# Performance work log

Hardware: AMD Instinct MI355X
Metric: run time of the kernel (lower is better)

## Reference

```python
import jax, jax.numpy as jnp
import numpy as np

N = 50000          # num nodes
E = 800000         # edges per adjacency
NUM_A = 4          # number of adjacency matrices
C = 2              # num_channels
D_IN = 128
D_OUT = 64


def setup_inputs() -> dict:
    key = jax.random.key(0)
    k1, k2, k3, k4, k5, k6 = jax.random.split(key, 6)
    H = jax.random.normal(k1, (N, D_IN), dtype=jnp.float32)
    vals = jax.random.uniform(k2, (NUM_A, E), dtype=jnp.float32)
    rows = jax.random.randint(k3, (NUM_A, E), 0, N, dtype=jnp.int32)
    cols = jax.random.randint(k4, (NUM_A, E), 0, N, dtype=jnp.int32)
    # xavier-ish init for learned params
    weight = jax.random.normal(k5, (C, D_IN, D_OUT), dtype=jnp.float32) * (2.0 / (D_IN + D_OUT)) ** 0.5
    att_weight = jax.random.normal(k6, (C, D_IN, NUM_A), dtype=jnp.float32) * (2.0 / (D_IN + NUM_A)) ** 0.5
    return {"H": H, "vals": vals, "weight": weight, "att_weight": att_weight,
            "rows": rows, "cols": cols}


def reference(H, vals, weight, att_weight, rows, cols):
    # H: [N, in], weight: [C, in, out], att_weight: [C, in, num_A]
    # rows/cols/vals: [num_A, E] COO edge lists for each sparse adjacency A_i
    n = H.shape[0]
    num_channels = weight.shape[0]
    Hc_all = jnp.einsum('nd,cdo->cno', H, weight)            # [C, N, out]
    score = jax.nn.softmax(att_weight.mean(axis=1), axis=1)   # [C, num_A]
    r = rows.reshape(-1)                                      # [num_A*E]
    cl = cols.reshape(-1)
    outs = []
    for c in range(num_channels):
        # A_combined = sum_i score[c, i] * A_i, applied as SpMM via segment_sum
        w = (score[c][:, None] * vals).reshape(-1)            # [num_A*E]
        msgs = Hc_all[c][cl] * w[:, None]                     # [num_A*E, out]
        outs.append(jax.ops.segment_sum(msgs, r, num_segments=n))
    return jnp.mean(jnp.stack(outs, axis=0), axis=0)          # [N, out]
```

## Files before the change

### kernel.cpp

```cpp
#include <hip/hip_runtime.h>
#include <hip/hip_fp16.h>

constexpr int D_IN  = 128;
constexpr int D_OUT = 64;
constexpr int NCH   = 2;
constexpr int NUM_A = 4;
constexpr int COLS  = NCH * D_OUT;
constexpr int RPB   = 64;
constexpr int MAXNB = 800;
constexpr int CAP   = 4608;
constexpr int SPT   = 512;
constexpr int RPT   = CAP / SPT;
constexpr int CAPB  = 6144;

typedef __attribute__((ext_vector_type(8))) short bf16x8;
typedef __attribute__((ext_vector_type(4))) float f32x4;

__device__ inline unsigned short f2bf_rn(float f) {
    unsigned u = __float_as_uint(f);
    return (unsigned short)((u + 0x7fffu + ((u >> 16) & 1u)) >> 16);
}
__device__ inline unsigned short f2h(float f) {
    _Float16 h = (_Float16)f;
    unsigned short u; __builtin_memcpy(&u, &h, 2); return u;
}
__device__ inline __half2 u2h2(unsigned u) {
    __half2 h; __builtin_memcpy(&h, &u, 4); return h;
}

__global__ __launch_bounds__(64) void score_kernel(const float* __restrict__ att,
                                                   float* __restrict__ score,
                                                   unsigned* __restrict__ cinit,
                                                   int NB, int padded) {
    int lane = threadIdx.x;
    for (int i = lane; i < NB; i += 64)
        cinit[i] = padded ? (unsigned)i * (unsigned)CAPB : 0u;
    int c = lane >> 2, a = lane & 3;
    float s = 0.0f;
    if (lane < 8) {
        const float* p = att + c * (D_IN * NUM_A) + a;
        for (int d = 0; d < D_IN; ++d) s += p[d * NUM_A];
        s *= (1.0f / D_IN);
    }
    float m = fmaxf(s, __shfl_xor(s, 1));
    m = fmaxf(m, __shfl_xor(m, 2));
    float ex = __expf(s - m);
    float sum = ex + __shfl_xor(ex, 1);
    sum += __shfl_xor(sum, 2);
    if (lane < 8) score[lane] = 0.5f * ex / sum;
}

__global__ __launch_bounds__(256) void gemm_kernel(const float* __restrict__ H,
                                                   const float* __restrict__ W,
                                                   unsigned short* __restrict__ Hc, int N) {
    __shared__ unsigned short Bs[128 * 136];

    const int t = threadIdx.x;
    for (int i = t; i < 128 * 128; i += 256) {
        const int k = i >> 7, n = i & 127;
        const int c = n >> 6, nn = n & 63;
        Bs[n * 136 + k] = f2bf_rn(W[c * (D_IN * D_OUT) + k * D_OUT + nn]);
    }

    const int lane = t & 63;
    const int wr   = t >> 6;
    const int kg   = lane >> 4;
    const int l15  = lane & 15;
    const int row0 = blockIdx.x * 64;

    int arow = row0 + wr * 16 + l15;
    if (arow >= N) arow = N - 1;

    bf16x8 afrag[4];
    const float* hrow = H + (size_t)arow * D_IN;
    #pragma unroll
    for (int s = 0; s < 4; ++s) {
        const int k0 = s * 32 + kg * 8;
        const float4 f0 = *reinterpret_cast<const float4*>(hrow + k0);
        const float4 f1 = *reinterpret_cast<const float4*>(hrow + k0 + 4);
        bf16x8 av;
        av[0] = (short)f2bf_rn(f0.x); av[1] = (short)f2bf_rn(f0.y);
        av[2] = (short)f2bf_rn(f0.z); av[3] = (short)f2bf_rn(f0.w);
        av[4] = (short)f2bf_rn(f1.x); av[5] = (short)f2bf_rn(f1.y);
        av[6] = (short)f2bf_rn(f1.z); av[7] = (short)f2bf_rn(f1.w);
        afrag[s] = av;
    }
    __syncthreads();

    #pragma unroll
    for (int nt = 0; nt < 8; ++nt) {
        const int n = nt * 16 + l15;
        f32x4 acc = {0.f, 0.f, 0.f, 0.f};
        #pragma unroll
        for (int s = 0; s < 4; ++s) {
            const bf16x8 bfrag =
                *reinterpret_cast<const bf16x8*>(&Bs[n * 136 + s * 32 + kg * 8]);
            acc = __builtin_amdgcn_mfma_f32_16x16x32_bf16(afrag[s], bfrag, acc, 0, 0, 0);
        }
        #pragma unroll
        for (int r = 0; r < 4; ++r) {
            const int drow = row0 + wr * 16 + kg * 4 + r;
            if (drow < N) Hc[(size_t)drow * COLS + n] = f2h(acc[r]);
        }
    }
}

__global__ __launch_bounds__(1024) void hist_kernel(const int* __restrict__ rows,
                                                    unsigned* __restrict__ counts,
                                                    int TE, int NB) {
    __shared__ unsigned h[MAXNB];
    const int t = threadIdx.x;
    for (int i = t; i < MAXNB; i += 1024) h[i] = 0u;
    __syncthreads();
    for (int e = blockIdx.x * 1024 + t; e < TE; e += gridDim.x * 1024)
        atomicAdd(&h[rows[e] >> 6], 1u);
    __syncthreads();
    for (int i = t; i < NB; i += 1024)
        if (h[i]) atomicAdd(&counts[i], h[i]);
}

__global__ __launch_bounds__(1024) void scan_kernel(const unsigned* __restrict__ counts,
                                                    unsigned* __restrict__ offsets,
                                                    unsigned* __restrict__ cursor, int n) {
    __shared__ unsigned part[1024];
    const int t = threadIdx.x;
    const int chunk = (n + 1023) >> 10;
    const int s = t * chunk;
    const int e = min(s + chunk, n);
    unsigned sum = 0;
    for (int i = s; i < e; ++i) sum += counts[i];
    part[t] = sum;
    __syncthreads();
    for (int d = 1; d < 1024; d <<= 1) {
        unsigned v = (t >= d) ? part[t - d] : 0u;
        __syncthreads();
        part[t] += v;
        __syncthreads();
    }
    unsigned run = (t == 0) ? 0u : part[t - 1];
    for (int i = s; i < e; ++i) {
        const unsigned c = counts[i];
        offsets[i] = run;
        cursor[i]  = run;
        run += c;
    }
}

constexpr int SC_T   = 1024;
constexpr int SC_EPT = 6;
constexpr int SC_CH  = SC_T * SC_EPT;

__global__ __launch_bounds__(SC_T) void scatter_kernel(const int* __restrict__ rows,
                                                       const int* __restrict__ cols,
                                                       const float* __restrict__ vals,
                                                       const float* __restrict__ score,
                                                       unsigned* __restrict__ cursor,
                                                       uint2* __restrict__ erec,
                                                       int TE, int Eper, int NB) {
    __shared__ unsigned lh[MAXNB];
    __shared__ unsigned lbase[MAXNB];
    __shared__ unsigned gbase[MAXNB];
    __shared__ unsigned wsum[16];
    __shared__ __align__(16) uint2 srec[SC_CH];
    __shared__ float ssc[8];

    const int t  = threadIdx.x;
    const int e0 = blockIdx.x * SC_CH;

    if (t < 8) ssc[t] = score[t];
    for (int i = t; i < MAXNB; i += SC_T) lh[i] = 0u;
    __syncthreads();

    unsigned bkrank[SC_EPT], meta[SC_EPT], wpk[SC_EPT];
    #pragma unroll
    for (int k = 0; k < SC_EPT; ++k) {
        const int e = e0 + k * SC_T + t;
        bkrank[k] = 0xffffffffu;
        if (e < TE) {
            const int row = rows[e];
            const int col = cols[e];
            const float v = vals[e];
            const int  a  = e / Eper;
            const unsigned bk = (unsigned)(row >> 6);
            const unsigned rk = atomicAdd(&lh[bk], 1u);
            bkrank[k] = (bk << 16) | rk;
            meta[k]   = (unsigned)col | ((unsigned)(row & 63) << 16) | (bk << 22);
            wpk[k]    = (unsigned)f2h(ssc[a] * v) |
                        ((unsigned)f2h(ssc[4 + a] * v) << 16);
        }
    }
    __syncthreads();

    const unsigned v = (t < NB) ? lh[t] : 0u;
    unsigned incl = v;
    #pragma unroll
    for (int d = 1; d < 64; d <<= 1) {
        const unsigned nb = __shfl_up(incl, d);
        if ((t & 63) >= d) incl += nb;
    }
    if ((t & 63) == 63) wsum[t >> 6] = incl;
    __syncthreads();
    if (t < 16) {
        const unsigned s = wsum[t];
        unsigned i2 = s;
        #pragma unroll
        for (int d = 1; d < 16; d <<= 1) {
            const unsigned nb = __shfl_up(i2, d);
            if (t >= d) i2 += nb;
        }
        wsum[t] = i2 - s;
    }
    __syncthreads();
    if (t < NB) {
        lbase[t] = incl - v + wsum[t >> 6];
        gbase[t] = v ? atomicAdd(&cursor[t], v) : 0u;
    }
    __syncthreads();

    #pragma unroll
    for (int k = 0; k < SC_EPT; ++k) {
        if (bkrank[k] != 0xffffffffu) {
            const unsigned p = lbase[bkrank[k] >> 16] + (bkrank[k] & 0xffffu);
            srec[p] = make_uint2(meta[k], wpk[k]);
        }
    }
    __syncthreads();

    const unsigned cn = min((unsigned)(TE - e0), (unsigned)SC_CH);
    #pragma unroll
    for (int k = 0; k < SC_EPT; ++k) {
        const unsigned p = (unsigned)(k * SC_T + t);
        if (p < cn) {
            const uint2 r = srec[p];
            const unsigned bk = r.x >> 22;
            const unsigned dst = gbase[bk] + (p - lbase[bk]);
            erec[dst] = make_uint2(r.x & 0x003fffffu, r.y);
        }
    }
}

__global__ __launch_bounds__(SPT) void bucketspmm_kernel(const uint2* __restrict__ erec,
                                                         const unsigned* __restrict__ offsets,
                                                         const unsigned* __restrict__ counts,
                                                         const unsigned* __restrict__ cursor,
                                                         const unsigned* __restrict__ Hc32,
                                                         float* __restrict__ out,
                                                         int N, int padded) {
    __shared__ __align__(16) uint2 srec[CAP];
    __shared__ unsigned roff8[8 * 68];
    __shared__ unsigned roff[RPB + 1];

    const int t    = threadIdx.x;
    const int lane = t & 63;
    const int w    = t >> 6;
    const int bucket = blockIdx.x;
    unsigned start, cnt;
    if (padded) {
        start = (unsigned)bucket * (unsigned)CAPB;
        cnt   = cursor[bucket] - start;
    } else {
        start = offsets[bucket];
        cnt   = counts[bucket];
    }
    const unsigned psel = (lane < 32) ? 0x01000100u : 0x03020302u;

    float2 acc[8];
    #pragma unroll
    for (int r = 0; r < 8; ++r) acc[r] = make_float2(0.f, 0.f);

    for (unsigned cb = 0; cb < cnt; cb += CAP) {
        const unsigned cn = min(cnt - cb, (unsigned)CAP);

        for (int i = t; i < 8 * 68; i += SPT) roff8[i] = 0u;
        __syncthreads();

        uint2 rec[RPT];
        unsigned rank[RPT];
        #pragma unroll
        for (int k = 0; k < RPT; ++k) {
            const unsigned idx = (unsigned)(k * SPT + t);
            rec[k] = make_uint2(0xffffffffu, 0u);
            if (idx < cn) {
                rec[k] = erec[start + cb + idx];
                rank[k] = atomicAdd(&roff8[w * 68 + (rec[k].x >> 16)], 1u);
            }
        }
        __syncthreads();

        if (t < 64) {
            unsigned run = 0;
            #pragma unroll
            for (int w2 = 0; w2 < 8; ++w2) {
                const unsigned v = roff8[w2 * 68 + t];
                roff8[w2 * 68 + t] = run;
                run += v;
            }
            unsigned incl = run;
            #pragma unroll
            for (int d = 1; d < 64; d <<= 1) {
                const unsigned nb = __shfl_up(incl, d);
                if (lane >= d) incl += nb;
            }
            roff[t] = incl - run;
            if (t == 63) roff[RPB] = incl;
        }
        __syncthreads();

        #pragma unroll
        for (int k = 0; k < RPT; ++k) {
            if (rec[k].x != 0xffffffffu) {
                const unsigned rib = rec[k].x >> 16;
                const unsigned pos = roff[rib] + roff8[w * 68 + rib] + rank[k];
                srec[pos] = make_uint2(rec[k].x & 0xffffu, rec[k].y);
            }
        }
        __syncthreads();

        #pragma unroll
        for (int rr = 0; rr < 8; ++rr) {
            const int r = w * 8 + rr;
            unsigned j = roff[r];
            const unsigned e = roff[r + 1];
            float2 a = acc[rr];

            while (j + 16 <= e) {
                unsigned hv16[16], wv16[16];
                #pragma unroll
                for (int k = 0; k < 16; ++k) {
                    const uint2 rc = srec[j + k];
                    hv16[k] = Hc32[(rc.x << 6) + lane];
                    wv16[k] = __builtin_amdgcn_perm(rc.y, rc.y, psel);
                }
                __half2 h2a = u2h2(0u), h2b = u2h2(0u);
                #pragma unroll
                for (int k = 0; k < 16; k += 2) {
                    h2a = __hfma2(u2h2(hv16[k]),     u2h2(wv16[k]),     h2a);
                    h2b = __hfma2(u2h2(hv16[k + 1]), u2h2(wv16[k + 1]), h2b);
                }
                const __half2 hs = __hadd2(h2a, h2b);
                a.x += __low2float(hs);
                a.y += __high2float(hs);
                j += 16;
            }
            if (j < e) {
                __half2 h2 = u2h2(0u);
                while (j + 4 <= e) {
                    unsigned hv4[4], wv4[4];
                    #pragma unroll
                    for (int k = 0; k < 4; ++k) {
                        const uint2 rc = srec[j + k];
                        hv4[k] = Hc32[(rc.x << 6) + lane];
                        wv4[k] = __builtin_amdgcn_perm(rc.y, rc.y, psel);
                    }
                    #pragma unroll
                    for (int k = 0; k < 4; ++k)
                        h2 = __hfma2(u2h2(hv4[k]), u2h2(wv4[k]), h2);
                    j += 4;
                }
                for (; j < e; ++j) {
                    const uint2 rc = srec[j];
                    const unsigned hv = Hc32[(rc.x << 6) + lane];
                    const unsigned wv = __builtin_amdgcn_perm(rc.y, rc.y, psel);
                    h2 = __hfma2(u2h2(hv), u2h2(wv), h2);
                }
                a.x += __low2float(h2);
                a.y += __high2float(h2);
            }
            acc[rr] = a;
        }
        __syncthreads();
    }

    const int row0 = bucket * RPB + w * 8;
    #pragma unroll
    for (int rr = 0; rr < 8; ++rr) {
        float2 a = acc[rr];
        a.x += __shfl_xor(a.x, 32);
        a.y += __shfl_xor(a.y, 32);
        const int row = row0 + rr;
        if (lane < 32 && row < N) {
            *reinterpret_cast<float2*>(out + (size_t)row * D_OUT + lane * 2) = a;
        }
    }
}

extern "C" void kernel_launch(void* const* d_in, const int* in_sizes, int n_in,
                              void* d_out, int out_size, void* d_ws, size_t ws_size,
                              hipStream_t stream) {
    const float* H    = (const float*)d_in[0];
    const float* vals = (const float*)d_in[1];
    const float* W    = (const float*)d_in[2];
    const float* att  = (const float*)d_in[3];
    const int*   rows = (const int*)d_in[4];
    const int*   cols = (const int*)d_in[5];

    const int N    = in_sizes[0] / D_IN;
    const int TE   = in_sizes[1];
    const int Eper = TE / NUM_A;
    const int NB   = (N + RPB - 1) / RPB;

    char* ws = (char*)d_ws;
    size_t off = 0;
    float* ws_score = (float*)(ws + off);          off += 256;
    unsigned short* ws_Hc = (unsigned short*)(ws + off);
    off += (size_t)N * COLS * sizeof(unsigned short);
    off = (off + 255) & ~(size_t)255;
    unsigned* counts  = (unsigned*)(ws + off);     off += (size_t)MAXNB * sizeof(unsigned);
    unsigned* offsets = (unsigned*)(ws + off);     off += (size_t)MAXNB * sizeof(unsigned);
    unsigned* cursor  = (unsigned*)(ws + off);     off += (size_t)MAXNB * sizeof(unsigned);
    off = (off + 255) & ~(size_t)255;
    uint2* erec       = (uint2*)(ws + off);

    const size_t need_padded = off + (size_t)NB * CAPB * sizeof(uint2);
    const int padded = (ws_size >= need_padded) ? 1 : 0;

    score_kernel<<<1, 64, 0, stream>>>(att, ws_score, padded ? cursor : counts,
                                       NB, padded);

    gemm_kernel<<<(N + 63) / 64, 256, 0, stream>>>(H, W, ws_Hc, N);

    if (!padded) {
        hist_kernel<<<512, 1024, 0, stream>>>(rows, counts, TE, NB);
        scan_kernel<<<1, 1024, 0, stream>>>(counts, offsets, cursor, NB);
    }

    const int sblocks = (TE + SC_CH - 1) / SC_CH;
    scatter_kernel<<<sblocks, SC_T, 0, stream>>>(rows, cols, vals, ws_score,
                                                 cursor, erec, TE, Eper, NB);

    bucketspmm_kernel<<<NB, SPT, 0, stream>>>(erec, offsets, counts, cursor,
                                              (const unsigned*)ws_Hc,
                                              (float*)d_out, N, padded);
}
```

Measured before the change: 233.4 us.

## Drop score kernel, fuse into gemm/scatter; vectorize SpMM gathers 16B per lane

Removes the separate score kernel: gemm block 0 initializes the cursor/count array, and each scatter block recomputes the softmax score itself. The SpMM inner loop is reorganized so each lane loads 16-byte (8 half) chunks of a gathered Hc row, and four edges are processed in parallel across lane quarters, with cross-lane shuffle reductions. Per-row results go through a shared-memory rowout buffer written out as float4. This cuts the number of gather load instructions and one launch, at the cost of extra shuffles, more LDS, a smaller chunk CAP and some redundant score computation in each scatter block.

Measured after the change: 239.0 us. 2.4% more time.

```diff
diff --git a/kernel.cpp b/kernel.cpp
--- a/kernel.cpp
+++ b/kernel.cpp
@@ -8,9 +8,10 @@
 constexpr int COLS  = NCH * D_OUT;
 constexpr int RPB   = 64;
 constexpr int MAXNB = 800;
-constexpr int CAP   = 4608;
+constexpr int CAP   = 4352;
+constexpr int CAPP  = CAP + 4;
 constexpr int SPT   = 512;
-constexpr int RPT   = CAP / SPT;
+constexpr int RPT   = 9;
 constexpr int CAPB  = 6144;
 
 typedef __attribute__((ext_vector_type(8))) short bf16x8;
@@ -28,34 +29,18 @@
     __half2 h; __builtin_memcpy(&h, &u, 4); return h;
 }
 
-__global__ __launch_bounds__(64) void score_kernel(const float* __restrict__ att,
-                                                   float* __restrict__ score,
-                                                   unsigned* __restrict__ cinit,
-                                                   int NB, int padded) {
-    int lane = threadIdx.x;
-    for (int i = lane; i < NB; i += 64)
-        cinit[i] = padded ? (unsigned)i * (unsigned)CAPB : 0u;
-    int c = lane >> 2, a = lane & 3;
-    float s = 0.0f;
-    if (lane < 8) {
-        const float* p = att + c * (D_IN * NUM_A) + a;
-        for (int d = 0; d < D_IN; ++d) s += p[d * NUM_A];
-        s *= (1.0f / D_IN);
-    }
-    float m = fmaxf(s, __shfl_xor(s, 1));
-    m = fmaxf(m, __shfl_xor(m, 2));
-    float ex = __expf(s - m);
-    float sum = ex + __shfl_xor(ex, 1);
-    sum += __shfl_xor(sum, 2);
-    if (lane < 8) score[lane] = 0.5f * ex / sum;
-}
-
 __global__ __launch_bounds__(256) void gemm_kernel(const float* __restrict__ H,
                                                    const float* __restrict__ W,
-                                                   unsigned short* __restrict__ Hc, int N) {
+                                                   unsigned short* __restrict__ Hc,
+                                                   unsigned* __restrict__ cinit,
+                                                   int N, int NB, int padded) {
     __shared__ unsigned short Bs[128 * 136];
 
     const int t = threadIdx.x;
+    if (blockIdx.x == 0) {
+        for (int i = t; i < NB; i += 256)
+            cinit[i] = padded ? (unsigned)i * (unsigned)CAPB : 0u;
+    }
     for (int i = t; i < 128 * 128; i += 256) {
         const int k = i >> 7, n = i & 127;
         const int c = n >> 6, nn = n & 63;
@@ -153,7 +138,7 @@
 __global__ __launch_bounds__(SC_T) void scatter_kernel(const int* __restrict__ rows,
                                                        const int* __restrict__ cols,
                                                        const float* __restrict__ vals,
-                                                       const float* __restrict__ score,
+                                                       const float* __restrict__ att,
                                                        unsigned* __restrict__ cursor,
                                                        uint2* __restrict__ erec,
                                                        int TE, int Eper, int NB) {
@@ -167,7 +152,22 @@
     const int t  = threadIdx.x;
     const int e0 = blockIdx.x * SC_CH;
 
-    if (t < 8) ssc[t] = score[t];
+    if (t < 64) {
+        const int lane = t;
+        int c = lane >> 2, a = lane & 3;
+        float s = 0.0f;
+        if (lane < 8) {
+            const float* p = att + c * (D_IN * NUM_A) + a;
+            for (int d = 0; d < D_IN; ++d) s += p[d * NUM_A];
+            s *= (1.0f / D_IN);
+        }
+        float m = fmaxf(s, __shfl_xor(s, 1));
+        m = fmaxf(m, __shfl_xor(m, 2));
+        float ex = __expf(s - m);
+        float sum = ex + __shfl_xor(ex, 1);
+        sum += __shfl_xor(sum, 2);
+        if (lane < 8) ssc[lane] = 0.5f * ex / sum;
+    }
     for (int i = t; i < MAXNB; i += SC_T) lh[i] = 0u;
     __syncthreads();
 
@@ -243,16 +243,19 @@
                                                          const unsigned* __restrict__ offsets,
                                                          const unsigned* __restrict__ counts,
                                                          const unsigned* __restrict__ cursor,
-                                                         const unsigned* __restrict__ Hc32,
+                                                         const unsigned short* __restrict__ Hc,
                                                          float* __restrict__ out,
                                                          int N, int padded) {
-    __shared__ __align__(16) uint2 srec[CAP];
+    __shared__ __align__(16) uint2 srec[CAPP];
     __shared__ unsigned roff8[8 * 68];
     __shared__ unsigned roff[RPB + 1];
+    __shared__ float rowout[RPB][D_OUT];
 
     const int t    = threadIdx.x;
     const int lane = t & 63;
     const int w    = t >> 6;
+    const int q    = lane >> 4;
+    const int il   = lane & 15;
     const int bucket = blockIdx.x;
     unsigned start, cnt;
     if (padded) {
@@ -262,12 +265,10 @@
         start = offsets[bucket];
         cnt   = counts[bucket];
     }
-    const unsigned psel = (lane < 32) ? 0x01000100u : 0x03020302u;
-
-    float2 acc[8];
-    #pragma unroll
-    for (int r = 0; r < 8; ++r) acc[r] = make_float2(0.f, 0.f);
-
+    const unsigned psel = (il < 8) ? 0x01000100u : 0x03020302u;
+    const unsigned short* Hcl = Hc + il * 8;
+
+    bool first_chunk = true;
     for (unsigned cb = 0; cb < cnt; cb += CAP) {
         const unsigned cn = min(cnt - cb, (unsigned)CAP);
 
@@ -291,9 +292,9 @@
             unsigned run = 0;
             #pragma unroll
             for (int w2 = 0; w2 < 8; ++w2) {
-                const unsigned v = roff8[w2 * 68 + t];
+                const unsigned vv = roff8[w2 * 68 + t];
                 roff8[w2 * 68 + t] = run;
-                run += v;
+                run += vv;
             }
             unsigned incl = run;
             #pragma unroll
@@ -314,6 +315,8 @@
                 srec[pos] = make_uint2(rec[k].x & 0xffffu, rec[k].y);
             }
         }
+        if (t < 4 && cn + (unsigned)t < (unsigned)CAPP)
+            srec[cn + t] = make_uint2(0u, 0u);
         __syncthreads();
 
         #pragma unroll
@@ -321,66 +324,73 @@
             const int r = w * 8 + rr;
             unsigned j = roff[r];
             const unsigned e = roff[r + 1];
-            float2 a = acc[rr];
+            __half2 a0 = u2h2(0u), a1 = u2h2(0u), a2 = u2h2(0u), a3 = u2h2(0u);
 
             while (j + 16 <= e) {
-                unsigned hv16[16], wv16[16];
                 #pragma unroll
-                for (int k = 0; k < 16; ++k) {
-                    const uint2 rc = srec[j + k];
-                    hv16[k] = Hc32[(rc.x << 6) + lane];
-                    wv16[k] = __builtin_amdgcn_perm(rc.y, rc.y, psel);
+                for (int b = 0; b < 4; ++b) {
+                    const uint2 rc = srec[j + b * 4 + q];
+                    const unsigned wv = __builtin_amdgcn_perm(rc.y, rc.y, psel);
+                    const uint4 hv = *reinterpret_cast<const uint4*>(
+                        Hcl + ((size_t)rc.x << 7));
+                    a0 = __hfma2(u2h2(hv.x), u2h2(wv), a0);
+                    a1 = __hfma2(u2h2(hv.y), u2h2(wv), a1);
+                    a2 = __hfma2(u2h2(hv.z), u2h2(wv), a2);
+                    a3 = __hfma2(u2h2(hv.w), u2h2(wv), a3);
                 }
-                __half2 h2a = u2h2(0u), h2b = u2h2(0u);
-                #pragma unroll
-                for (int k = 0; k < 16; k += 2) {
-                    h2a = __hfma2(u2h2(hv16[k]),     u2h2(wv16[k]),     h2a);
-                    h2b = __hfma2(u2h2(hv16[k + 1]), u2h2(wv16[k + 1]), h2b);
+                j += 16;
+            }
+            while (j < e) {
+                const uint2 rc = srec[j + q];
+                const unsigned wv = (j + (unsigned)q < e)
+                    ? __builtin_amdgcn_perm(rc.y, rc.y, psel) : 0u;
+                const uint4 hv = *reinterpret_cast<const uint4*>(
+                    Hcl + ((size_t)rc.x << 7));
+                a0 = __hfma2(u2h2(hv.x), u2h2(wv), a0);
+                a1 = __hfma2(u2h2(hv.y), u2h2(wv), a1);
+                a2 = __hfma2(u2h2(hv.z), u2h2(wv), a2);
+                a3 = __hfma2(u2h2(hv.w), u2h2(wv), a3);
+                j += 4;
+            }
+
+            float f[8];
+            f[0] = __low2float(a0); f[1] = __high2float(a0);
+            f[2] = __low2float(a1); f[3] = __high2float(a1);
+            f[4] = __low2float(a2); f[5] = __high2float(a2);
+            f[6] = __low2float(a3); f[7] = __high2float(a3);
+            #pragma unroll
+            for (int k = 0; k < 8; ++k) {
+                f[k] += __shfl_xor(f[k], 16);
+                f[k] += __shfl_xor(f[k], 32);
+                f[k] += __shfl_xor(f[k], 8);
+            }
+            if (lane < 8) {
+                float* ro = &rowout[r][lane * 8];
+                if (first_chunk) {
+                    #pragma unroll
+                    for (int k = 0; k < 8; ++k) ro[k] = f[k];
+                } else {
+                    #pragma unroll
+                    for (int k = 0; k < 8; ++k) ro[k] += f[k];
                 }
-                const __half2 hs = __hadd2(h2a, h2b);
-                a.x += __low2float(hs);
-                a.y += __high2float(hs);
-                j += 16;
-            }
-            if (j < e) {
-                __half2 h2 = u2h2(0u);
-                while (j + 4 <= e) {
-                    unsigned hv4[4], wv4[4];
-                    #pragma unroll
-                    for (int k = 0; k < 4; ++k) {
-                        const uint2 rc = srec[j + k];
-                        hv4[k] = Hc32[(rc.x << 6) + lane];
-                        wv4[k] = __builtin_amdgcn_perm(rc.y, rc.y, psel);
-                    }
-                    #pragma unroll
-                    for (int k = 0; k < 4; ++k)
-                        h2 = __hfma2(u2h2(hv4[k]), u2h2(wv4[k]), h2);
-                    j += 4;
-                }
-                for (; j < e; ++j) {
-                    const uint2 rc = srec[j];
-                    const unsigned hv = Hc32[(rc.x << 6) + lane];
-                    const unsigned wv = __builtin_amdgcn_perm(rc.y, rc.y, psel);
-                    h2 = __hfma2(u2h2(hv), u2h2(wv), h2);
-                }
-                a.x += __low2float(h2);
-                a.y += __high2float(h2);
-            }
-            acc[rr] = a;
-        }
-        __syncthreads();
-    }
-
-    const int row0 = bucket * RPB + w * 8;
-    #pragma unroll
-    for (int rr = 0; rr < 8; ++rr) {
-        float2 a = acc[rr];
-        a.x += __shfl_xor(a.x, 32);
-        a.y += __shfl_xor(a.y, 32);
-        const int row = row0 + rr;
-        if (lane < 32 && row < N) {
-            *reinterpret_cast<float2*>(out + (size_t)row * D_OUT + lane * 2) = a;
-        }
+            }
+        }
+        first_chunk = false;
+        __syncthreads();
+    }
+
+    if (cnt == 0) {
+        for (int i = t; i < RPB * D_OUT; i += SPT)
+            (&rowout[0][0])[i] = 0.0f;
+    }
+    __syncthreads();
+
+    const int row0 = bucket * RPB;
+    const float4* ro4 = reinterpret_cast<const float4*>(&rowout[0][0]);
+    for (int i = t; i < RPB * D_OUT / 4; i += SPT) {
+        const int row = row0 + (i >> 4);
+        if (row < N)
+            reinterpret_cast<float4*>(out + (size_t)row * D_OUT)[i & 15] = ro4[i];
     }
 }
 
@@ -401,7 +411,7 @@
 
     char* ws = (char*)d_ws;
     size_t off = 0;
-    float* ws_score = (float*)(ws + off);          off += 256;
+    off += 256;
     unsigned short* ws_Hc = (unsigned short*)(ws + off);
     off += (size_t)N * COLS * sizeof(unsigned short);
     off = (off + 255) & ~(size_t)255;
@@ -414,10 +424,9 @@
     const size_t need_padded = off + (size_t)NB * CAPB * sizeof(uint2);
     const int padded = (ws_size >= need_padded) ? 1 : 0;
 
-    score_kernel<<<1, 64, 0, stream>>>(att, ws_score, padded ? cursor : counts,
-                                       NB, padded);
-
-    gemm_kernel<<<(N + 63) / 64, 256, 0, stream>>>(H, W, ws_Hc, N);
+    gemm_kernel<<<(N + 63) / 64, 256, 0, stream>>>(H, W, ws_Hc,
+                                                   padded ? cursor : counts,
+                                                   N, NB, padded);
 
     if (!padded) {
         hist_kernel<<<512, 1024, 0, stream>>>(rows, counts, TE, NB);
@@ -425,10 +434,9 @@
     }
 
     const int sblocks = (TE + SC_CH - 1) / SC_CH;
-    scatter_kernel<<<sblocks, SC_T, 0, stream>>>(rows, cols, vals, ws_score,
+    scatter_kernel<<<sblocks, SC_T, 0, stream>>>(rows, cols, vals, att,
                                                  cursor, erec, TE, Eper, NB);
 
     bucketspmm_kernel<<<NB, SPT, 0, stream>>>(erec, offsets, counts, cursor,
-                                              (const unsigned*)ws_Hc,
-                                              (float*)d_out, N, padded);
-}
+                                              ws_Hc, (float*)d_out, N, padded);
+}
```
